# Optimization experiments

Measured on AMD Instinct MI355X. Metric: run time of the kernel, lower is better.

Reference implementation:

```python
import jax, jax.numpy as jnp
import numpy as np

B, N, M = 8, 8192, 2048
C1, C2 = 128, 256
H = 256  # mlp hidden/out channels


def setup_inputs() -> dict:
    key = jax.random.key(0)
    ks = jax.random.split(key, 8)
    return {
        "unknown": jax.random.normal(ks[0], (B, N, 3), dtype=jnp.float32),
        "known": jax.random.normal(ks[1], (B, M, 3), dtype=jnp.float32),
        "unknow_feats": jax.random.normal(ks[2], (B, C1, N), dtype=jnp.float32),
        "known_feats": jax.random.normal(ks[3], (B, C2, M), dtype=jnp.float32),
        "W1": jax.random.normal(ks[4], (H, C1 + C2), dtype=jnp.float32) * 0.02,
        "b1": jnp.zeros((H,), dtype=jnp.float32),
        "W2": jax.random.normal(ks[5], (H, H), dtype=jnp.float32) * 0.02,
        "b2": jnp.zeros((H,), dtype=jnp.float32),
    }


def _three_nn(unknown, known):
    # squared pairwise distances (B, n, m)
    d2 = jnp.sum((unknown[:, :, None, :] - known[:, None, :, :]) ** 2, axis=-1)
    neg_d2_top, idx = jax.lax.top_k(-d2, 3)  # 3 smallest distances
    dist = jnp.sqrt(jnp.maximum(-neg_d2_top, 0.0))  # (B, n, 3)
    return dist, idx


def _three_interpolate(features, idx, weight):
    # features: (B, c, m); idx, weight: (B, n, 3) -> (B, c, n)
    Bc, c, m = features.shape
    n = idx.shape[1]
    idx_flat = jnp.broadcast_to(idx.reshape(Bc, 1, n * 3), (Bc, c, n * 3))
    gathered = jnp.take_along_axis(features, idx_flat, axis=2).reshape(Bc, c, n, 3)
    return jnp.sum(gathered * weight[:, None, :, :], axis=-1)


def reference(unknown, known, unknow_feats, known_feats, W1, b1, W2, b2):
    dist, idx = _three_nn(unknown, known)
    dist_recip = 1.0 / (dist + 1e-8)
    weight = dist_recip / jnp.sum(dist_recip, axis=2, keepdims=True)  # (B, n, 3)
    interpolated = _three_interpolate(known_feats, idx, weight)  # (B, C2, n)
    new_features = jnp.concatenate([interpolated, unknow_feats], axis=1)  # (B, C1+C2, n)
    # shared MLP: two conv1x1 (bias, no BN) + ReLU
    h = jax.nn.relu(jnp.einsum('oc,bcn->bon', W1, new_features) + b1[None, :, None])
    out = jax.nn.relu(jnp.einsum('oc,bcn->bon', W2, h) + b2[None, :, None])
    return out
```

## Files before the change

### kernel.cpp

```cpp
#include <hip/hip_runtime.h>

using bf16x8 = __attribute__((ext_vector_type(8))) short;
using f32x4  = __attribute__((ext_vector_type(4))) float;

constexpr int Bb = 8, Nn = 8192, Mm = 2048, C1 = 128, C2 = 256, Hh = 256, K1 = 384;
constexpr int KT1 = K1 / 32;
constexpr int KT2 = Hh / 32;
constexpr int RT = Hh / 16;
constexpr int NTILES = Nn / 16;

__device__ __forceinline__ short f2bf(float x) {
  union { float f; unsigned u; } v; v.f = x;
  unsigned r = v.u + 0x7fff + ((v.u >> 16) & 1);
  return (short)(r >> 16);
}

__global__ __launch_bounds__(256) void transpose_k(const float* __restrict__ src,
                                                   float* __restrict__ dst, int R, int C) {
  __shared__ float tile[32][33];
  size_t off = (size_t)blockIdx.z * R * C;
  src += off; dst += off;
  int c0 = blockIdx.x * 32, r0 = blockIdx.y * 32;
  int tx = threadIdx.x, ty = threadIdx.y;
#pragma unroll
  for (int rr = ty; rr < 32; rr += 8) tile[rr][tx] = src[(size_t)(r0 + rr) * C + c0 + tx];
  __syncthreads();
#pragma unroll
  for (int cc = ty; cc < 32; cc += 8) dst[(size_t)(c0 + cc) * R + r0 + tx] = tile[tx][cc];
}

__global__ __launch_bounds__(256) void prep_w_k(const float* __restrict__ W1,
                                                const float* __restrict__ W2,
                                                short* __restrict__ W1f,
                                                short* __restrict__ W2f) {
  int id = blockIdx.x * 256 + threadIdx.x;
  const int n1 = KT1 * RT * 64;
  const int n2 = KT2 * RT * 64;
  if (id < n1) {
    int lane = id & 63, tile = id >> 6;
    int kt = tile / RT, rt = tile % RT;
    int m = rt * 16 + (lane & 15), k0 = kt * 32 + (lane >> 4) * 8;
    bf16x8 f;
#pragma unroll
    for (int j = 0; j < 8; ++j) f[j] = f2bf(W1[(size_t)m * K1 + k0 + j]);
    *(bf16x8*)(W1f + (size_t)id * 8) = f;
  } else if (id < n1 + n2) {
    int id2 = id - n1;
    int lane = id2 & 63, tile = id2 >> 6;
    int kt = tile / RT, rt = tile % RT;
    int m = rt * 16 + (lane & 15), k0 = kt * 32 + (lane >> 4) * 8;
    bf16x8 f;
#pragma unroll
    for (int j = 0; j < 8; ++j) f[j] = f2bf(W2[(size_t)m * Hh + k0 + j]);
    *(bf16x8*)(W2f + (size_t)id2 * 8) = f;
  }
}

__global__ __launch_bounds__(256) void nn_half_k(const float* __restrict__ unknown,
                                                 const float* __restrict__ known,
                                                 float* __restrict__ pd,
                                                 int* __restrict__ pi) {
  __shared__ float kx[1024], ky[1024], kz[1024];
  int bid = blockIdx.x;
  int b = bid >> 6, rem = bid & 63;
  int half = rem & 1, nblk = rem >> 1;
  int n = nblk * 256 + threadIdx.x;
  const float* kb = known + ((size_t)b * Mm + half * 1024) * 3;
  for (int p = threadIdx.x; p < 1024; p += 256) {
    kx[p] = kb[3 * p]; ky[p] = kb[3 * p + 1]; kz[p] = kb[3 * p + 2];
  }
  __syncthreads();

  size_t ui = ((size_t)b * Nn + n) * 3;
  float ux = unknown[ui], uy = unknown[ui + 1], uz = unknown[ui + 2];
  float d0 = 1e30f, d1 = 1e30f, d2 = 1e30f;
  int i0 = 0, i1 = 0, i2 = 0;
  int gbase = half * 1024;

#define NN_STEP(xx, yy, zz, q)                                          \
  {                                                                     \
    float dx = ux - (xx), dy = uy - (yy), dz = uz - (zz);               \
    float dd = dx * dx + dy * dy + dz * dz;                             \
    int jm = gbase + jb + (q);                                          \
    bool c0 = dd < d0, c1 = dd < d1, c2 = dd < d2;                      \
    d2 = c1 ? d1 : (c2 ? dd : d2); i2 = c1 ? i1 : (c2 ? jm : i2);       \
    d1 = c0 ? d0 : (c1 ? dd : d1); i1 = c0 ? i0 : (c1 ? jm : i1);       \
    d0 = c0 ? dd : d0;             i0 = c0 ? jm : i0;                   \
  }

  for (int jb = 0; jb < 1024; jb += 4) {
    float4 xs = *(const float4*)&kx[jb];
    float4 ys = *(const float4*)&ky[jb];
    float4 zs = *(const float4*)&kz[jb];
    NN_STEP(xs.x, ys.x, zs.x, 0)
    NN_STEP(xs.y, ys.y, zs.y, 1)
    NN_STEP(xs.z, ys.z, zs.z, 2)
    NN_STEP(xs.w, ys.w, zs.w, 3)
  }
#undef NN_STEP

  size_t o = (((size_t)b * Nn + n) * 2 + half) * 3;
  pd[o] = d0; pd[o + 1] = d1; pd[o + 2] = d2;
  pi[o] = i0; pi[o + 1] = i1; pi[o + 2] = i2;
}

__global__ __launch_bounds__(256) void nn_merge_k(const float* __restrict__ pd,
                                                  const int* __restrict__ pi,
                                                  int* __restrict__ idx3,
                                                  float* __restrict__ w3) {
  int t = blockIdx.x * 256 + threadIdx.x;
  size_t o = (size_t)t * 6;
  float a0 = pd[o], a1 = pd[o + 1], a2 = pd[o + 2];
  float b0 = pd[o + 3], b1v = pd[o + 4], b2v = pd[o + 5];
  int A0 = pi[o], A1 = pi[o + 1], A2 = pi[o + 2];
  int B0 = pi[o + 3], B1 = pi[o + 4], B2 = pi[o + 5];
  bool ta = a0 <= b0;
  float m0 = ta ? a0 : b0; int j0 = ta ? A0 : B0;
  float na0 = ta ? a1 : a0, na1 = ta ? a2 : a1;
  int   nA0 = ta ? A1 : A0, nA1 = ta ? A2 : A1;
  float nb0 = ta ? b0 : b1v, nb1 = ta ? b1v : b2v;
  int   nB0 = ta ? B0 : B1,  nB1 = ta ? B1 : B2;
  ta = na0 <= nb0;
  float m1 = ta ? na0 : nb0; int j1 = ta ? nA0 : nB0;
  float ma0 = ta ? na1 : na0; int mA0 = ta ? nA1 : nA0;
  float mb0 = ta ? nb0 : nb1; int mB0 = ta ? nB0 : nB1;
  ta = ma0 <= mb0;
  float m2 = ta ? ma0 : mb0; int j2 = ta ? mA0 : mB0;

  float s0 = sqrtf(m0), s1 = sqrtf(m1), s2 = sqrtf(m2);
  float r0 = 1.f / (s0 + 1e-8f), r1 = 1.f / (s1 + 1e-8f), r2 = 1.f / (s2 + 1e-8f);
  float rs = 1.f / (r0 + r1 + r2);
  size_t ui = (size_t)t * 3;
  idx3[ui] = j0; idx3[ui + 1] = j1; idx3[ui + 2] = j2;
  w3[ui] = r0 * rs; w3[ui + 1] = r1 * rs; w3[ui + 2] = r2 * rs;
}

__global__ __launch_bounds__(256) void gemm1_k(const float* __restrict__ uf,
                                               const float* __restrict__ kfT,
                                               const short* __restrict__ W1f,
                                               const float* __restrict__ b1,
                                               const int* __restrict__ idx3,
                                               const float* __restrict__ w3,
                                               short* __restrict__ hfrag) {
  __shared__ short Fs[KT1 * 4 * 64 * 8];
  int bid = blockIdx.x;
  int b = bid >> 7, bt = bid & 127;
  int tid = threadIdx.x, lane = tid & 63, wv = tid >> 6;
  int quad = lane >> 4, col = lane & 15;

  {
    int n = bt * 64 + wv * 16 + col;
    size_t o3 = ((size_t)b * Nn + n) * 3;
    int g0 = idx3[o3], g1 = idx3[o3 + 1], g2 = idx3[o3 + 2];
    float w0 = w3[o3], w1 = w3[o3 + 1], w2 = w3[o3 + 2];
    const float* kfb = kfT + (size_t)b * Mm * C2;
#pragma unroll 2
    for (int kt = 0; kt < 8; ++kt) {
      int c0 = kt * 32 + quad * 8;
      float4 p0a = *(const float4*)&kfb[(size_t)g0 * C2 + c0];
      float4 p0b = *(const float4*)&kfb[(size_t)g0 * C2 + c0 + 4];
      float4 p1a = *(const float4*)&kfb[(size_t)g1 * C2 + c0];
      float4 p1b = *(const float4*)&kfb[(size_t)g1 * C2 + c0 + 4];
      float4 p2a = *(const float4*)&kfb[(size_t)g2 * C2 + c0];
      float4 p2b = *(const float4*)&kfb[(size_t)g2 * C2 + c0 + 4];
      bf16x8 f;
      f[0] = f2bf(w0 * p0a.x + w1 * p1a.x + w2 * p2a.x);
      f[1] = f2bf(w0 * p0a.y + w1 * p1a.y + w2 * p2a.y);
      f[2] = f2bf(w0 * p0a.z + w1 * p1a.z + w2 * p2a.z);
      f[3] = f2bf(w0 * p0a.w + w1 * p1a.w + w2 * p2a.w);
      f[4] = f2bf(w0 * p0b.x + w1 * p1b.x + w2 * p2b.x);
      f[5] = f2bf(w0 * p0b.y + w1 * p1b.y + w2 * p2b.y);
      f[6] = f2bf(w0 * p0b.z + w1 * p1b.z + w2 * p2b.z);
      f[7] = f2bf(w0 * p0b.w + w1 * p1b.w + w2 * p2b.w);
      *(bf16x8*)&Fs[((kt * 4 + wv) * 64 + lane) * 8] = f;
    }
#pragma unroll 2
    for (int kt = 8; kt < 12; ++kt) {
      int c1 = (kt - 8) * 32 + quad * 8;
      bf16x8 f;
#pragma unroll
      for (int j = 0; j < 8; ++j)
        f[j] = f2bf(uf[((size_t)b * C1 + c1 + j) * Nn + n]);
      *(bf16x8*)&Fs[((kt * 4 + wv) * 64 + lane) * 8] = f;
    }
  }
  __syncthreads();

  f32x4 acc[4][4];
#pragma unroll
  for (int r = 0; r < 4; ++r)
#pragma unroll
    for (int c = 0; c < 4; ++c) acc[r][c] = (f32x4){0.f, 0.f, 0.f, 0.f};

  for (int kt = 0; kt < KT1; ++kt) {
    bf16x8 Afr[4], Bfr[4];
#pragma unroll
    for (int r = 0; r < 4; ++r)
      Afr[r] = *(const bf16x8*)(W1f + ((size_t)(kt * RT + wv * 4 + r) * 64 + lane) * 8);
#pragma unroll
    for (int c = 0; c < 4; ++c)
      Bfr[c] = *(const bf16x8*)&Fs[((kt * 4 + c) * 64 + lane) * 8];
#pragma unroll
    for (int r = 0; r < 4; ++r)
#pragma unroll
      for (int c = 0; c < 4; ++c)
        acc[r][c] = __builtin_amdgcn_mfma_f32_16x16x32_bf16(Afr[r], Bfr[c], acc[r][c], 0, 0, 0);
  }
  __syncthreads();

  float* sc = (float*)Fs + wv * 544;
  for (int ktl = 0; ktl < 2; ++ktl) {
    for (int c = 0; c < 4; ++c) {
#pragma unroll
      for (int r2 = 0; r2 < 2; ++r2) {
        int r = ktl * 2 + r2;
#pragma unroll
        for (int reg = 0; reg < 4; ++reg) {
          int rowg = wv * 64 + r * 16 + quad * 4 + reg;
          float hv = fmaxf(acc[r][c][reg] + b1[rowg], 0.f);
          sc[(r2 * 16 + quad * 4 + reg) * 17 + col] = hv;
        }
      }
      __syncthreads();
      bf16x8 f;
#pragma unroll
      for (int j = 0; j < 8; ++j) f[j] = f2bf(sc[(quad * 8 + j) * 17 + col]);
      int ktg = wv * 2 + ktl;
      int ntile = bt * 4 + c;
      *(bf16x8*)(hfrag + (((size_t)b * KT2 + ktg) * NTILES + ntile) * 64 * 8 + lane * 8) = f;
      __syncthreads();
    }
  }
}

__global__ __launch_bounds__(256) void gemm2_k(const short* __restrict__ W2f,
                                               const short* __restrict__ hfrag,
                                               const float* __restrict__ b2,
                                               float* __restrict__ out) {
  int bid = blockIdx.x;
  int b = bid >> 7, bt = bid & 127;
  int tid = threadIdx.x, lane = tid & 63, wv = tid >> 6;
  int quad = lane >> 4, col = lane & 15;

  f32x4 acc[4][4];
#pragma unroll
  for (int r = 0; r < 4; ++r)
#pragma unroll
    for (int c = 0; c < 4; ++c) acc[r][c] = (f32x4){0.f, 0.f, 0.f, 0.f};

  for (int kt = 0; kt < KT2; ++kt) {
    bf16x8 Afr[4], Bfr[4];
#pragma unroll
    for (int r = 0; r < 4; ++r)
      Afr[r] = *(const bf16x8*)(W2f + ((size_t)(kt * RT + wv * 4 + r) * 64 + lane) * 8);
#pragma unroll
    for (int c = 0; c < 4; ++c)
      Bfr[c] = *(const bf16x8*)(hfrag +
               (((size_t)b * KT2 + kt) * NTILES + bt * 4 + c) * 64 * 8 + lane * 8);
#pragma unroll
    for (int r = 0; r < 4; ++r)
#pragma unroll
      for (int c = 0; c < 4; ++c)
        acc[r][c] = __builtin_amdgcn_mfma_f32_16x16x32_bf16(Afr[r], Bfr[c], acc[r][c], 0, 0, 0);
  }

#pragma unroll
  for (int r = 0; r < 4; ++r)
#pragma unroll
    for (int c = 0; c < 4; ++c)
#pragma unroll
      for (int reg = 0; reg < 4; ++reg) {
        int rowg = wv * 64 + r * 16 + quad * 4 + reg;
        int n = bt * 64 + c * 16 + col;
        out[((size_t)b * Hh + rowg) * Nn + n] = fmaxf(acc[r][c][reg] + b2[rowg], 0.f);
      }
}

extern "C" void kernel_launch(void* const* d_in, const int* in_sizes, int n_in,
                              void* d_out, int out_size, void* d_ws, size_t ws_size,
                              hipStream_t stream) {
  const float* unknown = (const float*)d_in[0];
  const float* known   = (const float*)d_in[1];
  const float* uf      = (const float*)d_in[2];
  const float* kf      = (const float*)d_in[3];
  const float* W1      = (const float*)d_in[4];
  const float* b1      = (const float*)d_in[5];
  const float* W2      = (const float*)d_in[6];
  const float* b2      = (const float*)d_in[7];
  float* out = (float*)d_out;

  char* p = (char*)d_ws;
  float* kfT = (float*)p;  p += (size_t)Bb * Mm * C2 * 4;
  int* idx3  = (int*)p;    p += (size_t)Bb * Nn * 3 * 4;
  float* w3  = (float*)p;  p += (size_t)Bb * Nn * 3 * 4;
  short* W1f = (short*)p;  p += (size_t)KT1 * RT * 64 * 8 * 2;
  short* W2f = (short*)p;  p += (size_t)KT2 * RT * 64 * 8 * 2;
  short* hfrag = (short*)p; p += (size_t)Bb * KT2 * NTILES * 64 * 8 * 2;
  float* pd  = (float*)p;  p += (size_t)Bb * Nn * 2 * 3 * 4;
  int* pi    = (int*)p;    p += (size_t)Bb * Nn * 2 * 3 * 4;

  transpose_k<<<dim3(Mm / 32, C2 / 32, Bb), dim3(32, 8), 0, stream>>>(kf, kfT, C2, Mm);
  prep_w_k<<<dim3((KT1 * RT * 64 + KT2 * RT * 64) / 256), dim3(256), 0, stream>>>(W1, W2, W1f, W2f);
  nn_half_k<<<dim3(Bb * 64), dim3(256), 0, stream>>>(unknown, known, pd, pi);
  nn_merge_k<<<dim3(Bb * Nn / 256), dim3(256), 0, stream>>>(pd, pi, idx3, w3);
  gemm1_k<<<dim3(Bb * (Nn / 64)), dim3(256), 0, stream>>>(uf, kfT, W1f, b1, idx3, w3, hfrag);
  gemm2_k<<<dim3(Bb * (Nn / 64)), dim3(256), 0, stream>>>(W2f, hfrag, b2, out);
}
```

Measured before the change: 257.3 us.

## Fuse both MLP GEMMs via LDS and add wave-uniform skip in kNN scan

Merges the two MLP GEMM kernels into one. The ReLU'd hidden activations are converted to bf16 MFMA fragments with ds_bpermute and kept in shared memory, so the hfrag global round-trip and one launch go away. The kNN inner loop now skips the top-3 insertion when no lane in the wave has a closer candidate. Costs are extra LDS per block (Fs plus Hs), which may lower occupancy, and a branch per candidate in the NN scan.

```diff
diff --git a/kernel.cpp b/kernel.cpp
--- a/kernel.cpp
+++ b/kernel.cpp
@@ -7,7 +7,6 @@
 constexpr int KT1 = K1 / 32;
 constexpr int KT2 = Hh / 32;
 constexpr int RT = Hh / 16;
-constexpr int NTILES = Nn / 16;
 
 __device__ __forceinline__ short f2bf(float x) {
   union { float f; unsigned u; } v; v.f = x;
@@ -81,11 +80,13 @@
   {                                                                     \
     float dx = ux - (xx), dy = uy - (yy), dz = uz - (zz);               \
     float dd = dx * dx + dy * dy + dz * dz;                             \
-    int jm = gbase + jb + (q);                                          \
-    bool c0 = dd < d0, c1 = dd < d1, c2 = dd < d2;                      \
-    d2 = c1 ? d1 : (c2 ? dd : d2); i2 = c1 ? i1 : (c2 ? jm : i2);       \
-    d1 = c0 ? d0 : (c1 ? dd : d1); i1 = c0 ? i0 : (c1 ? jm : i1);       \
-    d0 = c0 ? dd : d0;             i0 = c0 ? jm : i0;                   \
+    if (__any(dd < d2)) {    \
+      int jm = gbase + jb + (q);                                        \
+      bool c0 = dd < d0, c1 = dd < d1, c2 = dd < d2;                    \
+      d2 = c1 ? d1 : (c2 ? dd : d2); i2 = c1 ? i1 : (c2 ? jm : i2);     \
+      d1 = c0 ? d0 : (c1 ? dd : d1); i1 = c0 ? i0 : (c1 ? jm : i1);     \
+      d0 = c0 ? dd : d0;             i0 = c0 ? jm : i0;                 \
+    }                                                                   \
   }
 
   for (int jb = 0; jb < 1024; jb += 4) {
@@ -135,14 +136,14 @@
   w3[ui] = r0 * rs; w3[ui + 1] = r1 * rs; w3[ui + 2] = r2 * rs;
 }
 
-__global__ __launch_bounds__(256) void gemm1_k(const float* __restrict__ uf,
-                                               const float* __restrict__ kfT,
-                                               const short* __restrict__ W1f,
-                                               const float* __restrict__ b1,
-                                               const int* __restrict__ idx3,
-                                               const float* __restrict__ w3,
-                                               short* __restrict__ hfrag) {
+__global__ __launch_bounds__(256) void fused_gemm_k(
+    const float* __restrict__ uf, const float* __restrict__ kfT,
+    const short* __restrict__ W1f, const float* __restrict__ b1,
+    const short* __restrict__ W2f, const float* __restrict__ b2,
+    const int* __restrict__ idx3, const float* __restrict__ w3,
+    float* __restrict__ out) {
   __shared__ short Fs[KT1 * 4 * 64 * 8];
+  __shared__ short Hs[KT2 * 4 * 64 * 8];
   int bid = blockIdx.x;
   int b = bid >> 7, bt = bid & 127;
   int tid = threadIdx.x, lane = tid & 63, wv = tid >> 6;
@@ -206,47 +207,41 @@
       for (int c = 0; c < 4; ++c)
         acc[r][c] = __builtin_amdgcn_mfma_f32_16x16x32_bf16(Afr[r], Bfr[c], acc[r][c], 0, 0, 0);
   }
+
+#pragma unroll
+  for (int r = 0; r < 4; ++r) {
+    f32x4 bq = *(const f32x4*)&b1[wv * 64 + r * 16 + quad * 4];
+#pragma unroll
+    for (int c = 0; c < 4; ++c)
+#pragma unroll
+      for (int reg = 0; reg < 4; ++reg)
+        acc[r][c][reg] = fmaxf(acc[r][c][reg] + bq[reg], 0.f);
+  }
+  {
+    int addr_lo = (((quad & 1) * 2) * 16 + col) * 4;
+    bool hiSel = lane >= 32;
+#pragma unroll
+    for (int ktl = 0; ktl < 2; ++ktl)
+#pragma unroll
+      for (int c = 0; c < 4; ++c) {
+        bf16x8 f;
+#pragma unroll
+        for (int j = 0; j < 8; ++j) {
+          int addr = addr_lo + (j >> 2) * 64;
+          int lo = __builtin_amdgcn_ds_bpermute(addr, __float_as_int(acc[ktl * 2][c][j & 3]));
+          int hi = __builtin_amdgcn_ds_bpermute(addr, __float_as_int(acc[ktl * 2 + 1][c][j & 3]));
+          f[j] = f2bf(__int_as_float(hiSel ? hi : lo));
+        }
+        *(bf16x8*)&Hs[(((wv * 2 + ktl) * 4 + c) * 64 + lane) * 8] = f;
+      }
+  }
   __syncthreads();
 
-  float* sc = (float*)Fs + wv * 544;
-  for (int ktl = 0; ktl < 2; ++ktl) {
-    for (int c = 0; c < 4; ++c) {
-#pragma unroll
-      for (int r2 = 0; r2 < 2; ++r2) {
-        int r = ktl * 2 + r2;
-#pragma unroll
-        for (int reg = 0; reg < 4; ++reg) {
-          int rowg = wv * 64 + r * 16 + quad * 4 + reg;
-          float hv = fmaxf(acc[r][c][reg] + b1[rowg], 0.f);
-          sc[(r2 * 16 + quad * 4 + reg) * 17 + col] = hv;
-        }
-      }
-      __syncthreads();
-      bf16x8 f;
-#pragma unroll
-      for (int j = 0; j < 8; ++j) f[j] = f2bf(sc[(quad * 8 + j) * 17 + col]);
-      int ktg = wv * 2 + ktl;
-      int ntile = bt * 4 + c;
-      *(bf16x8*)(hfrag + (((size_t)b * KT2 + ktg) * NTILES + ntile) * 64 * 8 + lane * 8) = f;
-      __syncthreads();
-    }
-  }
-}
-
-__global__ __launch_bounds__(256) void gemm2_k(const short* __restrict__ W2f,
-                                               const short* __restrict__ hfrag,
-                                               const float* __restrict__ b2,
-                                               float* __restrict__ out) {
-  int bid = blockIdx.x;
-  int b = bid >> 7, bt = bid & 127;
-  int tid = threadIdx.x, lane = tid & 63, wv = tid >> 6;
-  int quad = lane >> 4, col = lane & 15;
-
-  f32x4 acc[4][4];
+  f32x4 acc2[4][4];
 #pragma unroll
   for (int r = 0; r < 4; ++r)
 #pragma unroll
-    for (int c = 0; c < 4; ++c) acc[r][c] = (f32x4){0.f, 0.f, 0.f, 0.f};
+    for (int c = 0; c < 4; ++c) acc2[r][c] = (f32x4){0.f, 0.f, 0.f, 0.f};
 
   for (int kt = 0; kt < KT2; ++kt) {
     bf16x8 Afr[4], Bfr[4];
@@ -255,25 +250,26 @@
       Afr[r] = *(const bf16x8*)(W2f + ((size_t)(kt * RT + wv * 4 + r) * 64 + lane) * 8);
 #pragma unroll
     for (int c = 0; c < 4; ++c)
-      Bfr[c] = *(const bf16x8*)(hfrag +
-               (((size_t)b * KT2 + kt) * NTILES + bt * 4 + c) * 64 * 8 + lane * 8);
+      Bfr[c] = *(const bf16x8*)&Hs[((kt * 4 + c) * 64 + lane) * 8];
 #pragma unroll
     for (int r = 0; r < 4; ++r)
 #pragma unroll
       for (int c = 0; c < 4; ++c)
-        acc[r][c] = __builtin_amdgcn_mfma_f32_16x16x32_bf16(Afr[r], Bfr[c], acc[r][c], 0, 0, 0);
-  }
-
-#pragma unroll
-  for (int r = 0; r < 4; ++r)
+        acc2[r][c] = __builtin_amdgcn_mfma_f32_16x16x32_bf16(Afr[r], Bfr[c], acc2[r][c], 0, 0, 0);
+  }
+
+#pragma unroll
+  for (int r = 0; r < 4; ++r) {
+    f32x4 bq = *(const f32x4*)&b2[wv * 64 + r * 16 + quad * 4];
 #pragma unroll
     for (int c = 0; c < 4; ++c)
 #pragma unroll
       for (int reg = 0; reg < 4; ++reg) {
         int rowg = wv * 64 + r * 16 + quad * 4 + reg;
         int n = bt * 64 + c * 16 + col;
-        out[((size_t)b * Hh + rowg) * Nn + n] = fmaxf(acc[r][c][reg] + b2[rowg], 0.f);
+        out[((size_t)b * Hh + rowg) * Nn + n] = fmaxf(acc2[r][c][reg] + bq[reg], 0.f);
       }
+  }
 }
 
 extern "C" void kernel_launch(void* const* d_in, const int* in_sizes, int n_in,
@@ -295,7 +291,6 @@
   float* w3  = (float*)p;  p += (size_t)Bb * Nn * 3 * 4;
   short* W1f = (short*)p;  p += (size_t)KT1 * RT * 64 * 8 * 2;
   short* W2f = (short*)p;  p += (size_t)KT2 * RT * 64 * 8 * 2;
-  short* hfrag = (short*)p; p += (size_t)Bb * KT2 * NTILES * 64 * 8 * 2;
   float* pd  = (float*)p;  p += (size_t)Bb * Nn * 2 * 3 * 4;
   int* pi    = (int*)p;    p += (size_t)Bb * Nn * 2 * 3 * 4;
 
@@ -303,6 +298,6 @@
   prep_w_k<<<dim3((KT1 * RT * 64 + KT2 * RT * 64) / 256), dim3(256), 0, stream>>>(W1, W2, W1f, W2f);
   nn_half_k<<<dim3(Bb * 64), dim3(256), 0, stream>>>(unknown, known, pd, pi);
   nn_merge_k<<<dim3(Bb * Nn / 256), dim3(256), 0, stream>>>(pd, pi, idx3, w3);
-  gemm1_k<<<dim3(Bb * (Nn / 64)), dim3(256), 0, stream>>>(uf, kfT, W1f, b1, idx3, w3, hfrag);
-  gemm2_k<<<dim3(Bb * (Nn / 64)), dim3(256), 0, stream>>>(W2f, hfrag, b2, out);
-}
+  fused_gemm_k<<<dim3(Bb * (Nn / 64)), dim3(256), 0, stream>>>(
+      uf, kfT, W1f, b1, W2f, b2, idx3, w3, out);
+}
```

After: 241.1 us. 1.07x faster.
